# Performance work log

Hardware: AMD Instinct MI355X
Metric: run time of the kernel (lower is better)

The kernel has to match this reference:

```python
import jax, jax.numpy as jnp
import numpy as np

N_NODES = 100000
N_EDGES = 1_600_000
IN_CH = 128
HIDDEN = 128


def gcn_conv(x, src, dst, W, b):
    """PyG-style GCNConv: self-loops + symmetric deg^{-1/2} normalization."""
    n = x.shape[0]
    xw = x @ W  # [N, H]
    # degree on destination after adding self-loops (each node gets +1)
    deg = jax.ops.segment_sum(jnp.ones(src.shape[0], dtype=xw.dtype), dst,
                              num_segments=n) + 1.0
    dinv = jax.lax.rsqrt(deg)                      # deg^{-1/2}
    norm = dinv[src] * dinv[dst]                   # per-edge norm [E]
    agg = jax.ops.segment_sum(xw[src] * norm[:, None], dst, num_segments=n)
    # self-loop contribution: norm_ii = deg_i^{-1}
    return agg + xw * (1.0 / deg)[:, None] + b


def setup_inputs() -> dict:
    key = jax.random.key(0)
    ks = jax.random.split(key, 10)
    s = 0.05
    return {
        "node_features": jax.random.normal(ks[0], (N_NODES, IN_CH), dtype=jnp.float32),
        "edge_index": jax.random.randint(ks[1], (2, N_EDGES), 0, N_NODES, dtype=jnp.int32),
        "W1": jax.random.normal(ks[2], (IN_CH, HIDDEN), dtype=jnp.float32) * s,
        "b1": jnp.zeros((HIDDEN,), dtype=jnp.float32),
        "W2": jax.random.normal(ks[3], (HIDDEN, HIDDEN), dtype=jnp.float32) * s,
        "b2": jnp.zeros((HIDDEN,), dtype=jnp.float32),
        "fc1_w": jax.random.normal(ks[4], (2 * HIDDEN, HIDDEN), dtype=jnp.float32) * s,
        "fc1_b": jnp.zeros((HIDDEN,), dtype=jnp.float32),
        "fc2_w": jax.random.normal(ks[5], (HIDDEN, 1), dtype=jnp.float32) * s,
        "fc2_b": jnp.zeros((1,), dtype=jnp.float32),
    }


def reference(node_features, edge_index, W1, b1, W2, b2, fc1_w, fc1_b, fc2_w, fc2_b):
    src, dst = edge_index[0], edge_index[1]
    # two GCN layers (dropout is identity in eval mode)
    h = jax.nn.relu(gcn_conv(node_features, src, dst, W1, b1))
    h = jax.nn.relu(gcn_conv(h, src, dst, W2, b2))
    # edge feature head: gather endpoints, elementwise product/difference
    x = h[src]  # [E, H]
    y = h[dst]  # [E, H]
    edge_features = jnp.concatenate([x * y, x - y], axis=1)  # [E, 2H]
    z = jax.nn.relu(edge_features @ fc1_w + fc1_b)
    prob = jax.nn.sigmoid(z @ fc2_w + fc2_b)  # [E, 1]
    return prob
```

## Files before the change

kernel.cpp:

```cpp
#include <hip/hip_runtime.h>

#define THREADS 256

typedef __bf16    bf16x8 __attribute__((ext_vector_type(8)));
typedef _Float16  f16x8  __attribute__((ext_vector_type(8)));
typedef float     f32x4  __attribute__((ext_vector_type(4)));


__global__ __launch_bounds__(THREADS) void k_hist(const int* __restrict__ dst,
                                                  int* __restrict__ cnt, int E) {
    int e = blockIdx.x * THREADS + threadIdx.x;
    if (e < E) atomicAdd(&cnt[dst[e]], 1);
}

__global__ __launch_bounds__(THREADS) void k_scan1(const int* __restrict__ cnt,
                                                   int* __restrict__ rowptr,
                                                   int* __restrict__ blockSums,
                                                   float* __restrict__ dinv, int n) {
    __shared__ int part[THREADS];
    int tid = threadIdx.x;
    int base = blockIdx.x * 1024 + tid * 4;
    int v0 = (base + 0 < n) ? cnt[base + 0] : 0;
    int v1 = (base + 1 < n) ? cnt[base + 1] : 0;
    int v2 = (base + 2 < n) ? cnt[base + 2] : 0;
    int v3 = (base + 3 < n) ? cnt[base + 3] : 0;
    if (base + 0 < n) dinv[base + 0] = rsqrtf((float)v0 + 1.0f);
    if (base + 1 < n) dinv[base + 1] = rsqrtf((float)v1 + 1.0f);
    if (base + 2 < n) dinv[base + 2] = rsqrtf((float)v2 + 1.0f);
    if (base + 3 < n) dinv[base + 3] = rsqrtf((float)v3 + 1.0f);
    part[tid] = v0 + v1 + v2 + v3;
    __syncthreads();
    for (int off = 1; off < THREADS; off <<= 1) {
        int t = 0;
        if (tid >= off) t = part[tid - off];
        __syncthreads();
        if (tid >= off) part[tid] += t;
        __syncthreads();
    }
    int excl = (tid == 0) ? 0 : part[tid - 1];
    if (tid == THREADS - 1) blockSums[blockIdx.x] = part[THREADS - 1];
    int run = excl;
    if (base + 0 < n) rowptr[base + 0] = run; run += v0;
    if (base + 1 < n) rowptr[base + 1] = run; run += v1;
    if (base + 2 < n) rowptr[base + 2] = run; run += v2;
    if (base + 3 < n) rowptr[base + 3] = run;
}

__global__ __launch_bounds__(THREADS) void k_scan2(int* __restrict__ blockSums,
                                                   int* __restrict__ rowptr,
                                                   int nchunks, int n, int E) {
    __shared__ int part[THREADS];
    int tid = threadIdx.x;
    int v = (tid < nchunks) ? blockSums[tid] : 0;
    part[tid] = v;
    __syncthreads();
    for (int off = 1; off < THREADS; off <<= 1) {
        int t = 0;
        if (tid >= off) t = part[tid - off];
        __syncthreads();
        if (tid >= off) part[tid] += t;
        __syncthreads();
    }
    int excl = (tid == 0) ? 0 : part[tid - 1];
    if (tid < nchunks) blockSums[tid] = excl;
    if (tid == 0) rowptr[n] = E;
}

__global__ __launch_bounds__(THREADS) void k_scan3(int* __restrict__ rowptr,
                                                   const int* __restrict__ blockSums, int n) {
    int i = blockIdx.x * THREADS + threadIdx.x;
    if (i < n) rowptr[i] += blockSums[i >> 10];
}

__global__ __launch_bounds__(THREADS) void k_scatter(const int* __restrict__ src,
                                                     const int* __restrict__ dst,
                                                     const int* __restrict__ rowptr,
                                                     const float* __restrict__ dinv,
                                                     int* __restrict__ cursor,
                                                     int2* __restrict__ swPair,
                                                     int2* __restrict__ sdSorted,
                                                     int* __restrict__ edgePerm, int E) {
    int e = blockIdx.x * THREADS + threadIdx.x;
    if (e >= E) return;
    int d = dst[e];
    int s = src[e];
    int pos = rowptr[d] + atomicAdd(&cursor[d], 1);
    swPair[pos] = make_int2(s, __float_as_int(dinv[s]));
    sdSorted[pos] = make_int2(s, d);
    edgePerm[pos] = e;
}

__global__ __launch_bounds__(THREADS) void k_pack_w(const float* __restrict__ W1,
                                                    const float* __restrict__ W2,
                                                    _Float16* __restrict__ wp1,
                                                    _Float16* __restrict__ wp2) {
    int t = blockIdx.x * THREADS + threadIdx.x;
    const float* W = (t < 2048) ? W1 : W2;
    _Float16* wp = (t < 2048) ? wp1 : wp2;
    int tt = t & 2047;
    int lane = tt & 63;
    int fi = tt >> 6;
    int nt = fi & 7, ks = fi >> 3;
    int krow = ks * 32 + (lane >> 4) * 8;
    int col = nt * 16 + (lane & 15);
    f16x8 v;
#pragma unroll
    for (int i = 0; i < 8; i++) v[i] = (_Float16)W[(size_t)(krow + i) * 128 + col];
    *(f16x8*)(wp + (size_t)tt * 8) = v;
}

__global__ __launch_bounds__(THREADS) void k_gemm_mfma_f32(const float* __restrict__ A,
                                                           const _Float16* __restrict__ wpack,
                                                           __bf16* __restrict__ C16, int M) {
    __shared__ _Float16 wsh[2048 * 8];
    int tid = threadIdx.x;
    {
        const int4* g = (const int4*)wpack;
        int4* l = (int4*)wsh;
#pragma unroll
        for (int i = 0; i < 8; i++) l[tid + i * 256] = g[tid + i * 256];
    }
    int w = tid >> 6, lane = tid & 63;
    int m = lane & 15, kg = lane >> 4;
    int n0 = lane & 15, rowg = lane >> 4;
    int tile0 = blockIdx.x * 16 + w * 4;
    __syncthreads();
    const f16x8* wfr = ((const f16x8*)wsh) + lane;

    for (int t = 0; t < 4; t++) {
        int row = (tile0 + t) * 16 + m;
        f16x8 a[4];
        if (row < M) {
            const float* pa = A + (size_t)row * 128 + kg * 8;
#pragma unroll
            for (int ks = 0; ks < 4; ks++) {
                float4 lo = *(const float4*)(pa + ks * 32);
                float4 hi = *(const float4*)(pa + ks * 32 + 4);
                f16x8 v;
                v[0] = (_Float16)lo.x; v[1] = (_Float16)lo.y;
                v[2] = (_Float16)lo.z; v[3] = (_Float16)lo.w;
                v[4] = (_Float16)hi.x; v[5] = (_Float16)hi.y;
                v[6] = (_Float16)hi.z; v[7] = (_Float16)hi.w;
                a[ks] = v;
            }
        } else {
#pragma unroll
            for (int ks = 0; ks < 4; ks++) { f16x8 z = {}; a[ks] = z; }
        }
        f32x4 acc[8];
#pragma unroll
        for (int i = 0; i < 8; i++) acc[i] = (f32x4){0.f, 0.f, 0.f, 0.f};
#pragma unroll
        for (int ks = 0; ks < 4; ks++) {
#pragma unroll
            for (int nt = 0; nt < 8; nt++) {
                f16x8 b = wfr[(ks * 8 + nt) * 64];
                acc[nt] = __builtin_amdgcn_mfma_f32_16x16x32_f16(a[ks], b, acc[nt], 0, 0, 0);
            }
        }
#pragma unroll
        for (int nt = 0; nt < 8; nt++) {
#pragma unroll
            for (int r = 0; r < 4; r++) {
                int ro = (tile0 + t) * 16 + rowg * 4 + r;
                if (ro < M) C16[(size_t)ro * 128 + nt * 16 + n0] = (__bf16)acc[nt][r];
            }
        }
    }
}

__global__ __launch_bounds__(THREADS) void k_gemm_mfma_f16(const _Float16* __restrict__ A,
                                                           const _Float16* __restrict__ wpack,
                                                           __bf16* __restrict__ C16, int M) {
    __shared__ _Float16 wsh[2048 * 8];
    int tid = threadIdx.x;
    {
        const int4* g = (const int4*)wpack;
        int4* l = (int4*)wsh;
#pragma unroll
        for (int i = 0; i < 8; i++) l[tid + i * 256] = g[tid + i * 256];
    }
    int w = tid >> 6, lane = tid & 63;
    int m = lane & 15, kg = lane >> 4;
    int n0 = lane & 15, rowg = lane >> 4;
    int tile0 = blockIdx.x * 16 + w * 4;
    __syncthreads();
    const f16x8* wfr = ((const f16x8*)wsh) + lane;

    for (int t = 0; t < 4; t++) {
        int row = (tile0 + t) * 16 + m;
        f16x8 a[4];
        if (row < M) {
            const _Float16* pa = A + (size_t)row * 128 + kg * 8;
#pragma unroll
            for (int ks = 0; ks < 4; ks++) a[ks] = *(const f16x8*)(pa + ks * 32);
        } else {
#pragma unroll
            for (int ks = 0; ks < 4; ks++) { f16x8 z = {}; a[ks] = z; }
        }
        f32x4 acc[8];
#pragma unroll
        for (int i = 0; i < 8; i++) acc[i] = (f32x4){0.f, 0.f, 0.f, 0.f};
#pragma unroll
        for (int ks = 0; ks < 4; ks++) {
#pragma unroll
            for (int nt = 0; nt < 8; nt++) {
                f16x8 b = wfr[(ks * 8 + nt) * 64];
                acc[nt] = __builtin_amdgcn_mfma_f32_16x16x32_f16(a[ks], b, acc[nt], 0, 0, 0);
            }
        }
#pragma unroll
        for (int nt = 0; nt < 8; nt++) {
#pragma unroll
            for (int r = 0; r < 4; r++) {
                int ro = (tile0 + t) * 16 + rowg * 4 + r;
                if (ro < M) C16[(size_t)ro * 128 + nt * 16 + n0] = (__bf16)acc[nt][r];
            }
        }
    }
}

__global__ __launch_bounds__(THREADS) void k_gather_agg(const int* __restrict__ rowptr,
                                                        const int2* __restrict__ swPair,
                                                        const __bf16* __restrict__ xw16,
                                                        const float* __restrict__ dinv,
                                                        const float* __restrict__ bias,
                                                        _Float16* __restrict__ h16, int n) {
    int node = blockIdx.x * 4 + (threadIdx.x >> 6);
    int lane = threadIdx.x & 63;
    int q = lane >> 4;
    int c = lane & 15;
    if (node >= n) return;
    int beg = rowptr[node], end = rowptr[node + 1];
    float di = dinv[node];

    float acc[8];
#pragma unroll
    for (int i = 0; i < 8; i++) acc[i] = 0.f;

    int j = beg;
    for (; j + 15 < end; j += 16) {
        int2 pw0 = swPair[j + q];
        int2 pw1 = swPair[j + 4 + q];
        int2 pw2 = swPair[j + 8 + q];
        int2 pw3 = swPair[j + 12 + q];
        bf16x8 v0 = *(const bf16x8*)(xw16 + (size_t)pw0.x * 128 + c * 8);
        bf16x8 v1 = *(const bf16x8*)(xw16 + (size_t)pw1.x * 128 + c * 8);
        bf16x8 v2 = *(const bf16x8*)(xw16 + (size_t)pw2.x * 128 + c * 8);
        bf16x8 v3 = *(const bf16x8*)(xw16 + (size_t)pw3.x * 128 + c * 8);
        float w0 = __int_as_float(pw0.y);
        float w1 = __int_as_float(pw1.y);
        float w2 = __int_as_float(pw2.y);
        float w3 = __int_as_float(pw3.y);
#pragma unroll
        for (int i = 0; i < 8; i++) {
            acc[i] = fmaf((float)v0[i], w0, acc[i]);
            acc[i] = fmaf((float)v1[i], w1, acc[i]);
            acc[i] = fmaf((float)v2[i], w2, acc[i]);
            acc[i] = fmaf((float)v3[i], w3, acc[i]);
        }
    }
    for (; j + 7 < end; j += 8) {
        int2 pw0 = swPair[j + q];
        int2 pw1 = swPair[j + 4 + q];
        bf16x8 v0 = *(const bf16x8*)(xw16 + (size_t)pw0.x * 128 + c * 8);
        bf16x8 v1 = *(const bf16x8*)(xw16 + (size_t)pw1.x * 128 + c * 8);
        float w0 = __int_as_float(pw0.y);
        float w1 = __int_as_float(pw1.y);
#pragma unroll
        for (int i = 0; i < 8; i++) {
            acc[i] = fmaf((float)v0[i], w0, acc[i]);
            acc[i] = fmaf((float)v1[i], w1, acc[i]);
        }
    }
    for (; j + 3 < end; j += 4) {
        int2 pw = swPair[j + q];
        bf16x8 v = *(const bf16x8*)(xw16 + (size_t)pw.x * 128 + c * 8);
        float w = __int_as_float(pw.y);
#pragma unroll
        for (int i = 0; i < 8; i++) acc[i] = fmaf((float)v[i], w, acc[i]);
    }
    int rem = end - j;
    if (q < rem) {
        int2 pw = swPair[j + q];
        bf16x8 v = *(const bf16x8*)(xw16 + (size_t)pw.x * 128 + c * 8);
        float w = __int_as_float(pw.y);
#pragma unroll
        for (int i = 0; i < 8; i++) acc[i] = fmaf((float)v[i], w, acc[i]);
    }

#pragma unroll
    for (int i = 0; i < 8; i++) {
        acc[i] += __shfl_xor(acc[i], 16);
        acc[i] += __shfl_xor(acc[i], 32);
    }

    if (q == 0) {
        bf16x8 sv = *(const bf16x8*)(xw16 + (size_t)node * 128 + c * 8);
        float4 b0 = *(const float4*)(bias + c * 8);
        float4 b1 = *(const float4*)(bias + c * 8 + 4);
        float bb[8] = {b0.x, b0.y, b0.z, b0.w, b1.x, b1.y, b1.z, b1.w};
        float dd = di * di;
        f16x8 r16;
#pragma unroll
        for (int i = 0; i < 8; i++) {
            float r = fmaf(acc[i], di, fmaf((float)sv[i], dd, bb[i]));
            r16[i] = (_Float16)fmaxf(r, 0.f);
        }
        *(f16x8*)(h16 + (size_t)node * 128 + c * 8) = r16;
    }
}

__global__ __launch_bounds__(THREADS) void k_pack_b(const float* __restrict__ fc1w,
                                                    _Float16* __restrict__ bpack) {
    int t = blockIdx.x * THREADS + threadIdx.x;
    int lane = t & 63;
    int fi = t >> 6;
    int nt = fi & 7, ks = fi >> 3;
    int krow = ks * 32 + (lane >> 4) * 8;
    int col = nt * 16 + (lane & 15);
    f16x8 v;
#pragma unroll
    for (int i = 0; i < 8; i++) v[i] = (_Float16)fc1w[(size_t)(krow + i) * 128 + col];
    *(f16x8*)(bpack + (size_t)t * 8) = v;
}

__global__ __launch_bounds__(THREADS) void k_edge_head_mfma(const int2* __restrict__ sdSorted,
                                                            const int* __restrict__ edgePerm,
                                                            const _Float16* __restrict__ h16,
                                                            const _Float16* __restrict__ bpack,
                                                            const float* __restrict__ fc1b,
                                                            const float* __restrict__ fc2w,
                                                            const float* __restrict__ fc2b,
                                                            float* __restrict__ out, int E) {
    __shared__ _Float16 bsh[4096 * 8];

    int tid = threadIdx.x;
    {
        const int4* gsrc = (const int4*)bpack;
        int4* ldst = (int4*)bsh;
#pragma unroll
        for (int i = 0; i < 16; i++) ldst[tid + i * 256] = gsrc[tid + i * 256];
    }

    int w = tid >> 6;
    int lane = tid & 63;
    int m = lane & 15;
    int kg = lane >> 4;
    int n0 = lane & 15;
    int rowg = lane >> 4;
    int tile0 = blockIdx.x * 16 + w * 4;
    const f16x8* bfr = ((const f16x8*)bsh) + lane;
    float b2 = fc2b[0];

    float bb[8], ww[8];
#pragma unroll
    for (int nt = 0; nt < 8; nt++) {
        bb[nt] = fc1b[nt * 16 + n0];
        ww[nt] = fc2w[nt * 16 + n0];
    }

    auto LOAD = [&](int t, f16x8* xl, f16x8* yl) {
        int p = (tile0 + t) * 16 + m;
        int2 sd = (p < E) ? sdSorted[p] : make_int2(0, 0);
        const _Float16* px = h16 + (size_t)sd.x * 128 + kg * 8;
        const _Float16* py = h16 + (size_t)sd.y * 128 + kg * 8;
#pragma unroll
        for (int ks = 0; ks < 4; ks++) {
            xl[ks] = *(const f16x8*)(px + ks * 32);
            yl[ks] = *(const f16x8*)(py + ks * 32);
        }
    };

    auto COMPUTE = [&](int t, const f16x8* xl, const f16x8* yl) {
        f16x8 afrag[8];
#pragma unroll
        for (int ks = 0; ks < 4; ks++) {
            afrag[ks]     = xl[ks] * yl[ks];
            afrag[ks + 4] = xl[ks] - yl[ks];
        }
        f32x4 acc[8];
#pragma unroll
        for (int nt = 0; nt < 8; nt++) acc[nt] = (f32x4){bb[nt], bb[nt], bb[nt], bb[nt]};
#pragma unroll
        for (int ks = 0; ks < 8; ks++) {
#pragma unroll
            for (int nt = 0; nt < 8; nt++) {
                f16x8 b = bfr[(ks * 8 + nt) * 64];
                acc[nt] = __builtin_amdgcn_mfma_f32_16x16x32_f16(afrag[ks], b, acc[nt], 0, 0, 0);
            }
        }
        float partial[4] = {0.f, 0.f, 0.f, 0.f};
#pragma unroll
        for (int nt = 0; nt < 8; nt++) {
#pragma unroll
            for (int r = 0; r < 4; r++) {
                float z = fmaxf(acc[nt][r], 0.f);
                partial[r] = fmaf(z, ww[nt], partial[r]);
            }
        }
#pragma unroll
        for (int r = 0; r < 4; r++) {
            partial[r] += __shfl_xor(partial[r], 1);
            partial[r] += __shfl_xor(partial[r], 2);
            partial[r] += __shfl_xor(partial[r], 4);
            partial[r] += __shfl_xor(partial[r], 8);
        }
        if (n0 == 0) {
#pragma unroll
            for (int r = 0; r < 4; r++) {
                int qq = (tile0 + t) * 16 + rowg * 4 + r;
                if (qq < E) out[edgePerm[qq]] = 1.0f / (1.0f + expf(-(partial[r] + b2)));
            }
        }
    };

    f16x8 xa[4], ya[4], xb[4], yb[4];
    LOAD(0, xa, ya);
    __syncthreads();
    LOAD(1, xb, yb);
    COMPUTE(0, xa, ya);
    LOAD(2, xa, ya);
    COMPUTE(1, xb, yb);
    LOAD(3, xb, yb);
    COMPUTE(2, xa, ya);
    COMPUTE(3, xb, yb);
}

extern "C" void kernel_launch(void* const* d_in, const int* in_sizes, int n_in,
                              void* d_out, int out_size, void* d_ws, size_t ws_size,
                              hipStream_t stream) {
    const float* x    = (const float*)d_in[0];
    const int*   ei   = (const int*)d_in[1];
    const float* W1   = (const float*)d_in[2];
    const float* b1   = (const float*)d_in[3];
    const float* W2   = (const float*)d_in[4];
    const float* b2   = (const float*)d_in[5];
    const float* fc1w = (const float*)d_in[6];
    const float* fc1b = (const float*)d_in[7];
    const float* fc2w = (const float*)d_in[8];
    const float* fc2b = (const float*)d_in[9];

    int N = in_sizes[0] / 128;
    int E = in_sizes[1] / 2;
    const int* src = ei;
    const int* dst = ei + E;

    char* ws = (char*)d_ws;
    size_t off = 0;
    auto alloc = [&](size_t bytes) { char* p = ws + off; off += (bytes + 255) & ~(size_t)255; return p; };
    int*      cnt       = (int*)     alloc((size_t)N * 4);
    int*      rowptr    = (int*)     alloc(((size_t)N + 1) * 4);
    int*      cursor    = (int*)     alloc((size_t)N * 4);
    int*      blockSums = (int*)     alloc(256 * 4);
    int2*     swPair    = (int2*)    alloc((size_t)E * 8);
    int2*     sdSorted  = (int2*)    alloc((size_t)E * 8);
    int*      edgePerm  = (int*)     alloc((size_t)E * 4);
    float*    dinv      = (float*)   alloc((size_t)N * 4);
    _Float16* bpack     = (_Float16*)alloc((size_t)4096 * 8 * 2);
    _Float16* wp1       = (_Float16*)alloc((size_t)2048 * 8 * 2);
    _Float16* wp2       = (_Float16*)alloc((size_t)2048 * 8 * 2);
    __bf16*   xw16      = (__bf16*)  alloc((size_t)N * 128 * 2);
    _Float16* h16       = (_Float16*)alloc((size_t)N * 128 * 2);

    int gN     = (N + THREADS - 1) / THREADS;
    int gE     = (E + THREADS - 1) / THREADS;
    int nchunk = (N + 1023) / 1024;
    int nTileG = (N + 15) / 16;
    int gGemm  = (nTileG + 15) / 16;
    int gGath  = (N + 3) / 4;
    int gHead  = (E + 255) / 256;

    hipMemsetAsync(cnt, 0, (size_t)N * 4, stream);
    k_hist<<<gE, THREADS, 0, stream>>>(dst, cnt, E);
    k_scan1<<<nchunk, THREADS, 0, stream>>>(cnt, rowptr, blockSums, dinv, N);
    k_scan2<<<1, THREADS, 0, stream>>>(blockSums, rowptr, nchunk, N, E);
    k_scan3<<<gN, THREADS, 0, stream>>>(rowptr, blockSums, N);
    hipMemsetAsync(cursor, 0, (size_t)N * 4, stream);
    k_scatter<<<gE, THREADS, 0, stream>>>(src, dst, rowptr, dinv, cursor,
                                          swPair, sdSorted, edgePerm, E);
    k_pack_b<<<16, THREADS, 0, stream>>>(fc1w, bpack);
    k_pack_w<<<16, THREADS, 0, stream>>>(W1, W2, wp1, wp2);

    k_gemm_mfma_f32<<<gGemm, THREADS, 0, stream>>>(x, wp1, xw16, N);
    k_gather_agg<<<gGath, THREADS, 0, stream>>>(rowptr, swPair, xw16, dinv, b1, h16, N);

    k_gemm_mfma_f16<<<gGemm, THREADS, 0, stream>>>(h16, wp2, xw16, N);
    k_gather_agg<<<gGath, THREADS, 0, stream>>>(rowptr, swPair, xw16, dinv, b2, h16, N);

    k_edge_head_mfma<<<gHead, THREADS, 0, stream>>>(sdSorted, edgePerm,
                                                    h16, bpack, fc1b, fc2w, fc2b,
                                                    (float*)d_out, E);
}
```

Before: 492.8 us.

## Switch edge head to 32x32x16 MFMA tiles with repacked fc1 weights

```diff
diff --git a/kernel.cpp b/kernel.cpp
--- a/kernel.cpp
+++ b/kernel.cpp
@@ -5,6 +5,7 @@
 typedef __bf16    bf16x8 __attribute__((ext_vector_type(8)));
 typedef _Float16  f16x8  __attribute__((ext_vector_type(8)));
 typedef float     f32x4  __attribute__((ext_vector_type(4)));
+typedef float     f32x16 __attribute__((ext_vector_type(16)));
 
 
 __global__ __launch_bounds__(THREADS) void k_hist(const int* __restrict__ dst,
@@ -311,33 +312,34 @@
     }
 }
 
-__global__ __launch_bounds__(THREADS) void k_pack_b(const float* __restrict__ fc1w,
-                                                    _Float16* __restrict__ bpack) {
+__global__ __launch_bounds__(THREADS) void k_pack_b32(const float* __restrict__ fc1w,
+                                                      _Float16* __restrict__ bp) {
     int t = blockIdx.x * THREADS + threadIdx.x;
     int lane = t & 63;
     int fi = t >> 6;
-    int nt = fi & 7, ks = fi >> 3;
-    int krow = ks * 32 + (lane >> 4) * 8;
-    int col = nt * 16 + (lane & 15);
+    int nt = fi & 3, s = fi >> 2;
+    int krow = s * 16 + (lane >> 5) * 8;
+    int col = nt * 32 + (lane & 31);
     f16x8 v;
 #pragma unroll
     for (int i = 0; i < 8; i++) v[i] = (_Float16)fc1w[(size_t)(krow + i) * 128 + col];
-    *(f16x8*)(bpack + (size_t)t * 8) = v;
-}
-
-__global__ __launch_bounds__(THREADS) void k_edge_head_mfma(const int2* __restrict__ sdSorted,
-                                                            const int* __restrict__ edgePerm,
-                                                            const _Float16* __restrict__ h16,
-                                                            const _Float16* __restrict__ bpack,
-                                                            const float* __restrict__ fc1b,
-                                                            const float* __restrict__ fc2w,
-                                                            const float* __restrict__ fc2b,
-                                                            float* __restrict__ out, int E) {
+    *(f16x8*)(bp + (size_t)t * 8) = v;
+}
+
+__global__ __launch_bounds__(THREADS) void k_edge_head_mfma32(
+        const int2* __restrict__ sdSorted,
+        const int* __restrict__ edgePerm,
+        const _Float16* __restrict__ h16,
+        const _Float16* __restrict__ bpack32,
+        const float* __restrict__ fc1b,
+        const float* __restrict__ fc2w,
+        const float* __restrict__ fc2b,
+        float* __restrict__ out, int E) {
     __shared__ _Float16 bsh[4096 * 8];
 
     int tid = threadIdx.x;
     {
-        const int4* gsrc = (const int4*)bpack;
+        const int4* gsrc = (const int4*)bpack32;
         int4* ldst = (int4*)bsh;
 #pragma unroll
         for (int i = 0; i < 16; i++) ldst[tid + i * 256] = gsrc[tid + i * 256];
@@ -345,86 +347,80 @@
 
     int w = tid >> 6;
     int lane = tid & 63;
-    int m = lane & 15;
-    int kg = lane >> 4;
-    int n0 = lane & 15;
-    int rowg = lane >> 4;
-    int tile0 = blockIdx.x * 16 + w * 4;
+    int er = lane & 31;
+    int kh = (lane >> 5) * 8;
+    int col = lane & 31;
+    int half = lane >> 5;
     const f16x8* bfr = ((const f16x8*)bsh) + lane;
     float b2 = fc2b[0];
 
-    float bb[8], ww[8];
-#pragma unroll
-    for (int nt = 0; nt < 8; nt++) {
-        bb[nt] = fc1b[nt * 16 + n0];
-        ww[nt] = fc2w[nt * 16 + n0];
-    }
-
-    auto LOAD = [&](int t, f16x8* xl, f16x8* yl) {
-        int p = (tile0 + t) * 16 + m;
+    float bb[4], ww[4];
+#pragma unroll
+    for (int nt = 0; nt < 4; nt++) {
+        bb[nt] = fc1b[nt * 32 + col];
+        ww[nt] = fc2w[nt * 32 + col];
+    }
+
+    __syncthreads();
+
+    for (int tt = 0; tt < 2; tt++) {
+        int tile = blockIdx.x * 8 + w * 2 + tt;
+        int p = tile * 32 + er;
         int2 sd = (p < E) ? sdSorted[p] : make_int2(0, 0);
-        const _Float16* px = h16 + (size_t)sd.x * 128 + kg * 8;
-        const _Float16* py = h16 + (size_t)sd.y * 128 + kg * 8;
-#pragma unroll
-        for (int ks = 0; ks < 4; ks++) {
-            xl[ks] = *(const f16x8*)(px + ks * 32);
-            yl[ks] = *(const f16x8*)(py + ks * 32);
-        }
-    };
-
-    auto COMPUTE = [&](int t, const f16x8* xl, const f16x8* yl) {
-        f16x8 afrag[8];
-#pragma unroll
-        for (int ks = 0; ks < 4; ks++) {
-            afrag[ks]     = xl[ks] * yl[ks];
-            afrag[ks + 4] = xl[ks] - yl[ks];
-        }
-        f32x4 acc[8];
-#pragma unroll
-        for (int nt = 0; nt < 8; nt++) acc[nt] = (f32x4){bb[nt], bb[nt], bb[nt], bb[nt]};
-#pragma unroll
-        for (int ks = 0; ks < 8; ks++) {
-#pragma unroll
-            for (int nt = 0; nt < 8; nt++) {
-                f16x8 b = bfr[(ks * 8 + nt) * 64];
-                acc[nt] = __builtin_amdgcn_mfma_f32_16x16x32_f16(afrag[ks], b, acc[nt], 0, 0, 0);
-            }
-        }
-        float partial[4] = {0.f, 0.f, 0.f, 0.f};
-#pragma unroll
-        for (int nt = 0; nt < 8; nt++) {
-#pragma unroll
-            for (int r = 0; r < 4; r++) {
-                float z = fmaxf(acc[nt][r], 0.f);
-                partial[r] = fmaf(z, ww[nt], partial[r]);
-            }
-        }
-#pragma unroll
-        for (int r = 0; r < 4; r++) {
+        const _Float16* px = h16 + (size_t)sd.x * 128 + kh;
+        const _Float16* py = h16 + (size_t)sd.y * 128 + kh;
+
+        f32x16 acc[4];
+#pragma unroll
+        for (int nt = 0; nt < 4; nt++) {
+#pragma unroll
+            for (int r = 0; r < 16; r++) acc[nt][r] = bb[nt];
+        }
+
+#pragma unroll
+        for (int s = 0; s < 8; s++) {
+            f16x8 xv = *(const f16x8*)(px + s * 16);
+            f16x8 yv = *(const f16x8*)(py + s * 16);
+            f16x8 pa = xv * yv;
+            f16x8 pd = xv - yv;
+#pragma unroll
+            for (int nt = 0; nt < 4; nt++) {
+                f16x8 bA = bfr[(s * 4 + nt) * 64];
+                acc[nt] = __builtin_amdgcn_mfma_f32_32x32x16_f16(pa, bA, acc[nt], 0, 0, 0);
+            }
+#pragma unroll
+            for (int nt = 0; nt < 4; nt++) {
+                f16x8 bB = bfr[((s + 8) * 4 + nt) * 64];
+                acc[nt] = __builtin_amdgcn_mfma_f32_32x32x16_f16(pd, bB, acc[nt], 0, 0, 0);
+            }
+        }
+
+        float partial[16];
+#pragma unroll
+        for (int r = 0; r < 16; r++) {
+            float sum = fmaxf(acc[0][r], 0.f) * ww[0];
+            sum = fmaf(fmaxf(acc[1][r], 0.f), ww[1], sum);
+            sum = fmaf(fmaxf(acc[2][r], 0.f), ww[2], sum);
+            sum = fmaf(fmaxf(acc[3][r], 0.f), ww[3], sum);
+            partial[r] = sum;
+        }
+#pragma unroll
+        for (int r = 0; r < 16; r++) {
             partial[r] += __shfl_xor(partial[r], 1);
             partial[r] += __shfl_xor(partial[r], 2);
             partial[r] += __shfl_xor(partial[r], 4);
             partial[r] += __shfl_xor(partial[r], 8);
-        }
-        if (n0 == 0) {
-#pragma unroll
-            for (int r = 0; r < 4; r++) {
-                int qq = (tile0 + t) * 16 + rowg * 4 + r;
+            partial[r] += __shfl_xor(partial[r], 16);
+        }
+        if (col == 0) {
+#pragma unroll
+            for (int r = 0; r < 16; r++) {
+                int row = (r & 3) + 8 * (r >> 2) + 4 * half;
+                int qq = tile * 32 + row;
                 if (qq < E) out[edgePerm[qq]] = 1.0f / (1.0f + expf(-(partial[r] + b2)));
             }
         }
-    };
-
-    f16x8 xa[4], ya[4], xb[4], yb[4];
-    LOAD(0, xa, ya);
-    __syncthreads();
-    LOAD(1, xb, yb);
-    COMPUTE(0, xa, ya);
-    LOAD(2, xa, ya);
-    COMPUTE(1, xb, yb);
-    LOAD(3, xb, yb);
-    COMPUTE(2, xa, ya);
-    COMPUTE(3, xb, yb);
+    }
 }
 
 extern "C" void kernel_launch(void* const* d_in, const int* in_sizes, int n_in,
@@ -457,7 +453,7 @@
     int2*     sdSorted  = (int2*)    alloc((size_t)E * 8);
     int*      edgePerm  = (int*)     alloc((size_t)E * 4);
     float*    dinv      = (float*)   alloc((size_t)N * 4);
-    _Float16* bpack     = (_Float16*)alloc((size_t)4096 * 8 * 2);
+    _Float16* bpack32   = (_Float16*)alloc((size_t)4096 * 8 * 2);
     _Float16* wp1       = (_Float16*)alloc((size_t)2048 * 8 * 2);
     _Float16* wp2       = (_Float16*)alloc((size_t)2048 * 8 * 2);
     __bf16*   xw16      = (__bf16*)  alloc((size_t)N * 128 * 2);
@@ -479,7 +475,7 @@
     hipMemsetAsync(cursor, 0, (size_t)N * 4, stream);
     k_scatter<<<gE, THREADS, 0, stream>>>(src, dst, rowptr, dinv, cursor,
                                           swPair, sdSorted, edgePerm, E);
-    k_pack_b<<<16, THREADS, 0, stream>>>(fc1w, bpack);
+    k_pack_b32<<<16, THREADS, 0, stream>>>(fc1w, bpack32);
     k_pack_w<<<16, THREADS, 0, stream>>>(W1, W2, wp1, wp2);
 
     k_gemm_mfma_f32<<<gGemm, THREADS, 0, stream>>>(x, wp1, xw16, N);
@@ -488,7 +484,7 @@
     k_gemm_mfma_f16<<<gGemm, THREADS, 0, stream>>>(h16, wp2, xw16, N);
     k_gather_agg<<<gGath, THREADS, 0, stream>>>(rowptr, swPair, xw16, dinv, b2, h16, N);
 
-    k_edge_head_mfma<<<gHead, THREADS, 0, stream>>>(sdSorted, edgePerm,
-                                                    h16, bpack, fc1b, fc2w, fc2b,
-                                                    (float*)d_out, E);
-}
+    k_edge_head_mfma32<<<gHead, THREADS, 0, stream>>>(sdSorted, edgePerm,
+                                                      h16, bpack32, fc1b, fc2w, fc2b,
+                                                      (float*)d_out, E);
+}
```

Measured after the change: 815.3 us. 65.4% more time.
